# Performance work log

Hardware: AMD Instinct MI355X
Metric: run time of the kernel (lower is better)

## Reference

```python
import jax, jax.numpy as jnp
import numpy as np

B, N, CS, CV, K = 8, 2048, 256, 128, 3
EPS = 1e-6


def _eq_layernorm(s, v):
    # scalars: standard layernorm over channels; vectors: RMS of channel norms (equivariant)
    mu = s.mean(-1, keepdims=True)
    var = ((s - mu) ** 2).mean(-1, keepdims=True)
    s = (s - mu) * jax.lax.rsqrt(var + EPS)
    n2 = (v ** 2).sum(-1).mean(-1, keepdims=True)  # [b,n,1]
    v = v * jax.lax.rsqrt(n2 + EPS)[..., None]
    return s, v


def setup_inputs() -> dict:
    key = jax.random.key(0)
    ks = jax.random.split(key, 7)
    fan_s = K * (CS + CV)       # 1152
    fan_v = K * (CS + 2 * CV)   # 1536
    return {
        "x_s": jax.random.normal(ks[0], (B, N, CS), jnp.float32),
        "x_v": jax.random.normal(ks[1], (B, N, CV, 3), jnp.float32),
        "coords": jax.random.normal(ks[2], (B, N, 3), jnp.float32) * 10.0,
        "W_conv_s": jax.random.normal(ks[3], (fan_s, CS), jnp.float32),
        "W_conv_v": jax.random.normal(ks[4], (fan_v, CV), jnp.float32),
        "W_si_s": jax.random.normal(ks[5], (CS, CS), jnp.float32),
        "W_si_v": jax.random.normal(ks[6], (CV, CV), jnp.float32),
    }


def reference(x_s, x_v, coords, W_conv_s, W_conv_v, W_si_s, W_si_v):
    b, n, cs = x_s.shape
    cv = x_v.shape[2]
    pad = K // 2
    # 'same' padding: zeros for features, edge for coords (zero displacement at boundary)
    sp = jnp.pad(x_s, ((0, 0), (pad, pad), (0, 0)))
    vp = jnp.pad(x_v, ((0, 0), (pad, pad), (0, 0), (0, 0)))
    cp = jnp.pad(coords, ((0, 0), (pad, pad), (0, 0)), mode="edge")
    s_win = jnp.stack([sp[:, k:k + n] for k in range(K)], 2)   # [b,n,K,cs]
    v_win = jnp.stack([vp[:, k:k + n] for k in range(K)], 2)   # [b,n,K,cv,3]
    c_win = jnp.stack([cp[:, k:k + n] for k in range(K)], 2)   # [b,n,K,3]

    d = c_win - coords[:, :, None, :]
    dn = jnp.linalg.norm(d, axis=-1, keepdims=True)
    rhat = d * jnp.where(dn > 1e-6, 1.0 / jnp.maximum(dn, 1e-6), 0.0)

    # Clebsch-Gordan paths of (0e,1e) features with sh = (1, rhat)
    vdot = jnp.einsum("bnkcd,bnkd->bnkc", v_win, rhat)                    # 1x1 -> 0
    scal_in = jnp.concatenate([s_win, vdot], -1).reshape(b, n, -1)        # [b,n,K*(cs+cv)]
    s_rhat = s_win[..., None] * rhat[:, :, :, None, :]                    # 0x1 -> 1
    v_cross = jnp.cross(v_win, rhat[:, :, :, None, :])                    # 1x1 -> 1
    vec_in = jnp.concatenate([v_win, s_rhat, v_cross], 3).reshape(b, n, -1, 3)

    # SequenceConvolution linear mixing (fan-in normalized) + norm=True
    h_s = jnp.einsum("bnp,po->bno", scal_in, W_conv_s) / float(np.sqrt(scal_in.shape[-1]))
    h_v = jnp.einsum("bnpd,po->bnod", vec_in, W_conv_v) / float(np.sqrt(vec_in.shape[2]))
    h_s, h_v = _eq_layernorm(h_s, h_v)

    # SelfInteraction: per-degree channel mixing, residual=True, norm_last=True
    y_s = h_s + h_s @ W_si_s / float(np.sqrt(cs))
    y_v = h_v + jnp.einsum("bncd,co->bnod", h_v, W_si_v) / float(np.sqrt(cv))
    y_s, y_v = _eq_layernorm(y_s, y_v)

    # block Residual + final EquivariantLayerNorm
    z_s, z_v = _eq_layernorm(x_s + y_s, x_v + y_v)
    return z_s, z_v
```

## Files before the change

kernel.cpp:

```cpp
#include <hip/hip_runtime.h>
#include <hip/hip_bf16.h>


typedef __attribute__((ext_vector_type(8))) short short8;
typedef __attribute__((ext_vector_type(4))) short short4v;
typedef __attribute__((ext_vector_type(4))) float f32x4;
typedef unsigned short u16;

#define B_   8
#define N_   2048
#define EPS_ 1e-6f
#define TB   32

#define OFF_CS 0
#define OFF_V  294912
#define OFF_G  393216
#define OFF_SS 491520
#define OFF_SV 557056

#define MFMA(a,b,c) __builtin_amdgcn_mfma_f32_16x16x32_bf16((a),(b),(c),0,0,0)

__device__ __forceinline__ u16 f2b(float v){ __hip_bfloat16 h=__float2bfloat16(v); return *(u16*)&h; }

__global__ __launch_bounds__(256) void prep_weights(
    const float* __restrict__ Wcs, const float* __restrict__ Wcv,
    const float* __restrict__ Wss, const float* __restrict__ Wsv,
    u16* __restrict__ ws)
{
    const int bid = blockIdx.x;
    const float* src; int N, r0, ld, c0; u16* dst; int tile;
    if (bid < 288)      { src=Wcs; N=256; r0=0; dst=ws+OFF_CS; ld=1152; c0=0; tile=bid; }
    else if (bid < 336) { int k=(bid-288)/16; tile=(bid-288)%16;
                          src=Wcv; N=128; r0=k*512;     dst=ws+OFF_V; ld=768; c0=k*256; }
    else if (bid < 432) { int k=(bid-336)/32; tile=(bid-336)%32;
                          src=Wcv; N=128; r0=k*512+128; dst=ws+OFF_G; ld=768; c0=k*256; }
    else if (bid < 480) { int k=(bid-432)/16; tile=(bid-432)%16;
                          src=Wcv; N=128; r0=k*512+384; dst=ws+OFF_V; ld=768; c0=k*256+128; }
    else if (bid < 544) { tile=bid-480; src=Wss; N=256; r0=0; dst=ws+OFF_SS; ld=256; c0=0; }
    else                { tile=bid-544; src=Wsv; N=128; r0=0; dst=ws+OFF_SV; ld=128; c0=0; }
    const int ntN = N >> 5;
    const int kt = (tile/ntN)*32, nn = (tile%ntN)*32;
    __shared__ float t[32][33];
    const int r = threadIdx.x >> 5, c = threadIdx.x & 31;
#pragma unroll
    for (int i = 0; i < 4; ++i)
        t[r+8*i][c] = src[(size_t)(r0+kt+r+8*i)*N + nn+c];
    __syncthreads();
#pragma unroll
    for (int i = 0; i < 4; ++i)
        dst[(size_t)(nn+r+8*i)*ld + c0+kt+c] = f2b(t[c][r+8*i]);
}

__device__ __forceinline__ void ln_reduce8(
    float p1[2][4], float p2[2][4], float pv[2][4], f32x4* red,
    int lm, int lq4, int w, float mu[2][4], float ss[2][4], float vs[2][4])
{
    __syncthreads();
#pragma unroll
    for (int m2 = 1; m2 < 16; m2 <<= 1)
#pragma unroll
        for (int m = 0; m < 2; ++m)
#pragma unroll
            for (int q = 0; q < 4; ++q) {
                p1[m][q] += __shfl_xor(p1[m][q], m2);
                p2[m][q] += __shfl_xor(p2[m][q], m2);
                pv[m][q] += __shfl_xor(pv[m][q], m2);
            }
    if (lm == 0)
#pragma unroll
        for (int m = 0; m < 2; ++m)
#pragma unroll
            for (int q = 0; q < 4; ++q) {
                f32x4 r = {p1[m][q], p2[m][q], pv[m][q], 0.f};
                red[(m*16+lq4+q)*8 + w] = r;
            }
    __syncthreads();
#pragma unroll
    for (int m = 0; m < 2; ++m)
#pragma unroll
        for (int q = 0; q < 4; ++q) {
            const int t = m*16 + lq4 + q;
            f32x4 rs = red[t*8+0];
#pragma unroll
            for (int i = 1; i < 8; ++i) rs += red[t*8+i];
            const float mm = rs.x * (1.f/256.f);
            mu[m][q] = mm;
            ss[m][q] = rsqrtf(rs.y*(1.f/256.f) - mm*mm + EPS_);
            vs[m][q] = rsqrtf(rs.z*(1.f/128.f) + EPS_);
        }
}

__global__ __launch_bounds__(512, 2) void mixing_main(
    const float* __restrict__ x_s, const float* __restrict__ x_v,
    const float* __restrict__ coords, const u16* __restrict__ wt,
    float* __restrict__ out)
{
    __shared__ __align__(16) char smem[81408];
    u16* fs  = (u16*)smem;
    u16* fv  = (u16*)(smem + 25088);
    u16* hsb = (u16*)smem;
    u16* hvb = (u16*)(smem + 25088);
    float* xvL = (float*)(smem + 25088);
    float* rhp = (float*)(smem + 75776);
    f32x4* red = (f32x4*)(smem + 77312);

    const int tid = threadIdx.x;
    const int w   = tid >> 6, l = tid & 63;
    const int lm  = l & 15, lk8 = (l >> 4) << 3, lq4 = (l >> 4) << 2;
    const int gt0 = blockIdx.x * TB;
    const int n0  = gt0 & (N_ - 1);
    const int seq0 = gt0 - n0;
    const size_t ZV0 = (size_t)B_ * N_ * 256;

    if (tid < 96) {
        const int t = tid / 3, k = tid - 3 * (tid / 3);
        const int jn = n0 + t + k - 1;
        const int jc = jn < 0 ? 0 : (jn > N_-1 ? N_-1 : jn);
        const float* cj = coords + (size_t)(seq0 + jc) * 3;
        const float* c0p = coords + (size_t)(gt0 + t) * 3;
        const float d0 = cj[0]-c0p[0], d1 = cj[1]-c0p[1], d2 = cj[2]-c0p[2];
        const float dn = sqrtf(d0*d0 + d1*d1 + d2*d2);
        const float inv = dn > 1e-6f ? 1.f/dn : 0.f;
        rhp[(t*3+k)*4+0] = d0*inv; rhp[(t*3+k)*4+1] = d1*inv; rhp[(t*3+k)*4+2] = d2*inv;
    }
    __syncthreads();

    const f32x4 fz = {0.f,0.f,0.f,0.f};
    f32x4 acc_s[2][2] = {{fz,fz},{fz,fz}};
    f32x4 accv[6] = {fz,fz,fz,fz,fz,fz};
    f32x4 agc[2] = {fz, fz};

    const int bt = tid >> 4;
    const int bx = tid & 15;

#pragma unroll
    for (int k = 0; k < 3; ++k) {
        const int jn = n0 + bt + k - 1;
        const bool valid = (unsigned)jn < (unsigned)N_;
        const size_t j = (size_t)seq0 + (valid ? jn : 0);
        {
            const int c0 = bx * 16;
            float v[16];
            if (valid) {
                const float4* sp = (const float4*)(x_s + j*256 + c0);
#pragma unroll
                for (int i = 0; i < 4; ++i) {
                    float4 f = sp[i];
                    v[4*i]=f.x; v[4*i+1]=f.y; v[4*i+2]=f.z; v[4*i+3]=f.w;
                }
            } else {
#pragma unroll
                for (int i = 0; i < 16; ++i) v[i] = 0.f;
            }
            short8 p0, p1;
#pragma unroll
            for (int i = 0; i < 8; ++i) { p0[i]=(short)f2b(v[i]); p1[i]=(short)f2b(v[8+i]); }
            *(short8*)(fs + bt*392 + c0)     = p0;
            *(short8*)(fs + bt*392 + c0 + 8) = p1;
        }
        {
            const int c0 = bx * 8;
            const float r0 = rhp[(bt*3+k)*4+0];
            const float r1 = rhp[(bt*3+k)*4+1];
            const float r2 = rhp[(bt*3+k)*4+2];
#pragma unroll
            for (int hh = 0; hh < 2; ++hh) {
                float vv[12];
                if (valid) {
                    const float4* vp = (const float4*)(x_v + ((size_t)j*128 + c0 + 4*hh)*3);
#pragma unroll
                    for (int i = 0; i < 3; ++i) {
                        float4 f = vp[i];
                        vv[4*i]=f.x; vv[4*i+1]=f.y; vv[4*i+2]=f.z; vv[4*i+3]=f.w;
                    }
                } else {
#pragma unroll
                    for (int i = 0; i < 12; ++i) vv[i] = 0.f;
                }
                short4v dv, w0, w1, w2, x0, x1, x2;
#pragma unroll
                for (int m = 0; m < 4; ++m) {
                    const float a0 = vv[3*m], a1 = vv[3*m+1], a2 = vv[3*m+2];
                    dv[m] = (short)f2b(a0*r0 + a1*r1 + a2*r2);
                    w0[m] = (short)f2b(a0); w1[m] = (short)f2b(a1); w2[m] = (short)f2b(a2);
                    x0[m] = (short)f2b(a1*r2 - a2*r1);
                    x1[m] = (short)f2b(a2*r0 - a0*r2);
                    x2[m] = (short)f2b(a0*r1 - a1*r0);
                }
                const int cc = c0 + 4*hh;
                *(short4v*)(fs + bt*392 + 256 + cc)          = dv;
                *(short4v*)(fv + (0*32+bt)*264 + cc)         = w0;
                *(short4v*)(fv + (1*32+bt)*264 + cc)         = w1;
                *(short4v*)(fv + (2*32+bt)*264 + cc)         = w2;
                *(short4v*)(fv + (0*32+bt)*264 + 128 + cc)   = x0;
                *(short4v*)(fv + (1*32+bt)*264 + 128 + cc)   = x1;
                *(short4v*)(fv + (2*32+bt)*264 + 128 + cc)   = x2;
            }
        }

        const u16* bS0 = wt + OFF_CS + k*384 + (size_t)((2*w+0)*16+lm)*1152;
        const u16* bS1 = wt + OFF_CS + k*384 + (size_t)((2*w+1)*16+lm)*1152;
        const u16* bGp = wt + OFF_G  + k*256 + (size_t)(w*16+lm)*768;
        const u16* bVp = wt + OFF_V  + k*256 + (size_t)(w*16+lm)*768;
        short8 Bs0[3], Bs1[3], Bg[3], Bv[4];
#pragma unroll
        for (int i = 0; i < 3; ++i) {
            Bs0[i] = *(const short8*)(bS0 + i*32 + lk8);
            Bs1[i] = *(const short8*)(bS1 + i*32 + lk8);
            Bg[i]  = *(const short8*)(bGp + i*32 + lk8);
        }
        __syncthreads();

#pragma unroll
        for (int ks = 0; ks < 12; ++ks) {
            const int r = ks % 3;
            const short8 b0 = Bs0[r], b1 = Bs1[r], bg = Bg[r];
            if (ks + 3 < 12) {
                Bs0[r] = *(const short8*)(bS0 + (ks+3)*32 + lk8);
                Bs1[r] = *(const short8*)(bS1 + (ks+3)*32 + lk8);
            }
            if (ks + 3 < 8)
                Bg[r] = *(const short8*)(bGp + (ks+3)*32 + lk8);
            if (ks == 9) {
#pragma unroll
                for (int i = 0; i < 4; ++i)
                    Bv[i] = *(const short8*)(bVp + i*32 + lk8);
            }
            const int ko = ks*32 + lk8;
            const short8 a0 = *(const short8*)(fs + lm*392 + ko);
            const short8 a1 = *(const short8*)(fs + (16+lm)*392 + ko);
            acc_s[0][0] = MFMA(a0, b0, acc_s[0][0]);
            acc_s[1][0] = MFMA(a1, b0, acc_s[1][0]);
            acc_s[0][1] = MFMA(a0, b1, acc_s[0][1]);
            acc_s[1][1] = MFMA(a1, b1, acc_s[1][1]);
            if (ks < 8) {
                agc[0] = MFMA(a0, bg, agc[0]);
                agc[1] = MFMA(a1, bg, agc[1]);
            }
        }
#pragma unroll
        for (int ks = 0; ks < 8; ++ks) {
            const int r = ks & 3;
            const short8 bv = Bv[r];
            if (ks + 4 < 8)
                Bv[r] = *(const short8*)(bVp + (ks+4)*32 + lk8);
            const int ko = ks*32 + lk8;
#pragma unroll
            for (int mi = 0; mi < 6; ++mi) {
                const short8 a = *(const short8*)(fv + (mi*16+lm)*264 + ko);
                accv[mi] = MFMA(a, bv, accv[mi]);
            }
        }
#pragma unroll
        for (int mi = 0; mi < 6; ++mi) {
            const int m = mi & 1, d = mi >> 1;
#pragma unroll
            for (int q = 0; q < 4; ++q)
                accv[mi][q] += agc[m][q] * rhp[((m*16+lq4+q)*3 + k)*4 + d];
        }
        agc[0] = fz; agc[1] = fz;
        __syncthreads();
    }

    const float inv_fs = 0.029462783f;
    const float inv_fv = 0.0255155136f;
#pragma unroll
    for (int m = 0; m < 2; ++m)
#pragma unroll
        for (int u = 0; u < 2; ++u)
#pragma unroll
            for (int q = 0; q < 4; ++q) acc_s[m][u][q] *= inv_fs;
#pragma unroll
    for (int mi = 0; mi < 6; ++mi)
#pragma unroll
        for (int q = 0; q < 4; ++q) accv[mi][q] *= inv_fv;

    float p1[2][4], p2[2][4], pv[2][4], mu[2][4], ss[2][4], vs[2][4];
#pragma unroll
    for (int m = 0; m < 2; ++m)
#pragma unroll
        for (int q = 0; q < 4; ++q) {
            float a = 0.f, b = 0.f, c = 0.f;
#pragma unroll
            for (int u = 0; u < 2; ++u) { const float x = acc_s[m][u][q]; a += x; b += x*x; }
#pragma unroll
            for (int d = 0; d < 3; ++d) { const float x = accv[d*2+m][q]; c += x*x; }
            p1[m][q] = a; p2[m][q] = b; pv[m][q] = c;
        }
    ln_reduce8(p1, p2, pv, red, lm, lq4, w, mu, ss, vs);

#pragma unroll
    for (int m = 0; m < 2; ++m)
#pragma unroll
        for (int u = 0; u < 2; ++u)
#pragma unroll
            for (int q = 0; q < 4; ++q) {
                const float h = (acc_s[m][u][q] - mu[m][q]) * ss[m][q];
                acc_s[m][u][q] = h;
                hsb[(m*16+lq4+q)*264 + (2*w+u)*16 + lm] = f2b(h);
            }
#pragma unroll
    for (int mi = 0; mi < 6; ++mi)
#pragma unroll
        for (int q = 0; q < 4; ++q) {
            const float h = accv[mi][q] * vs[mi&1][q];
            accv[mi][q] = h;
            hvb[(mi*16+lq4+q)*136 + w*16 + lm] = f2b(h);
        }

    const u16* bP0 = wt + OFF_SS + (size_t)((2*w+0)*16+lm)*256;
    const u16* bP1 = wt + OFF_SS + (size_t)((2*w+1)*16+lm)*256;
    const u16* bPv = wt + OFF_SV + (size_t)(w*16+lm)*128;
    short8 Cs0[3], Cs1[3], Cv[4];
#pragma unroll
    for (int i = 0; i < 3; ++i) {
        Cs0[i] = *(const short8*)(bP0 + i*32 + lk8);
        Cs1[i] = *(const short8*)(bP1 + i*32 + lk8);
    }
#pragma unroll
    for (int i = 0; i < 4; ++i)
        Cv[i] = *(const short8*)(bPv + i*32 + lk8);
    __syncthreads();

    f32x4 accs[2][2] = {{fz,fz},{fz,fz}};
    f32x4 accw[6] = {fz,fz,fz,fz,fz,fz};
#pragma unroll
    for (int ks = 0; ks < 8; ++ks) {
        const int r = ks % 3;
        const short8 c0 = Cs0[r], c1 = Cs1[r];
        if (ks + 3 < 8) {
            Cs0[r] = *(const short8*)(bP0 + (ks+3)*32 + lk8);
            Cs1[r] = *(const short8*)(bP1 + (ks+3)*32 + lk8);
        }
        const int ko = ks*32 + lk8;
        const short8 a0 = *(const short8*)(hsb + lm*264 + ko);
        const short8 a1 = *(const short8*)(hsb + (16+lm)*264 + ko);
        accs[0][0] = MFMA(a0, c0, accs[0][0]);
        accs[1][0] = MFMA(a1, c0, accs[1][0]);
        accs[0][1] = MFMA(a0, c1, accs[0][1]);
        accs[1][1] = MFMA(a1, c1, accs[1][1]);
    }
#pragma unroll
    for (int ks = 0; ks < 4; ++ks) {
        const int ko = ks*32 + lk8;
#pragma unroll
        for (int mi = 0; mi < 6; ++mi) {
            const short8 a = *(const short8*)(hvb + (mi*16+lm)*136 + ko);
            accw[mi] = MFMA(a, Cv[ks], accw[mi]);
        }
    }

#pragma unroll
    for (int m = 0; m < 2; ++m)
#pragma unroll
        for (int u = 0; u < 2; ++u)
#pragma unroll
            for (int q = 0; q < 4; ++q) acc_s[m][u][q] += accs[m][u][q] * 0.0625f;
#pragma unroll
    for (int mi = 0; mi < 6; ++mi)
#pragma unroll
        for (int q = 0; q < 4; ++q) accv[mi][q] += accw[mi][q] * 0.08838834764f;

#pragma unroll
    for (int m = 0; m < 2; ++m)
#pragma unroll
        for (int q = 0; q < 4; ++q) {
            float a = 0.f, b = 0.f, c = 0.f;
#pragma unroll
            for (int u = 0; u < 2; ++u) { const float x = acc_s[m][u][q]; a += x; b += x*x; }
#pragma unroll
            for (int d = 0; d < 3; ++d) { const float x = accv[d*2+m][q]; c += x*x; }
            p1[m][q] = a; p2[m][q] = b; pv[m][q] = c;
        }
    float4 xr[6];
    {
        const float4* xvsrc = (const float4*)(x_v + (size_t)gt0 * 384);
#pragma unroll
        for (int i = 0; i < 6; ++i) xr[i] = xvsrc[tid + i*512];
    }
    ln_reduce8(p1, p2, pv, red, lm, lq4, w, mu, ss, vs);
#pragma unroll
    for (int i = 0; i < 6; ++i) ((float4*)xvL)[tid + i*512] = xr[i];
    __syncthreads();

#pragma unroll
    for (int m = 0; m < 2; ++m)
#pragma unroll
        for (int u = 0; u < 2; ++u)
#pragma unroll
            for (int q = 0; q < 4; ++q)
                acc_s[m][u][q] = (acc_s[m][u][q] - mu[m][q]) * ss[m][q]
                    + x_s[(size_t)(gt0 + m*16 + lq4 + q)*256 + (2*w+u)*16 + lm];
#pragma unroll
    for (int mi = 0; mi < 6; ++mi)
#pragma unroll
        for (int q = 0; q < 4; ++q) {
            const int t = (mi&1)*16 + lq4 + q;
            accv[mi][q] = accv[mi][q] * vs[mi&1][q]
                + xvL[t*384 + (w*16+lm)*3 + (mi>>1)];
        }

#pragma unroll
    for (int m = 0; m < 2; ++m)
#pragma unroll
        for (int q = 0; q < 4; ++q) {
            float a = 0.f, b = 0.f, c = 0.f;
#pragma unroll
            for (int u = 0; u < 2; ++u) { const float x = acc_s[m][u][q]; a += x; b += x*x; }
#pragma unroll
            for (int d = 0; d < 3; ++d) { const float x = accv[d*2+m][q]; c += x*x; }
            p1[m][q] = a; p2[m][q] = b; pv[m][q] = c;
        }
    ln_reduce8(p1, p2, pv, red, lm, lq4, w, mu, ss, vs);

#pragma unroll
    for (int m = 0; m < 2; ++m)
#pragma unroll
        for (int u = 0; u < 2; ++u)
#pragma unroll
            for (int q = 0; q < 4; ++q)
                out[(size_t)(gt0 + m*16 + lq4 + q)*256 + (2*w+u)*16 + lm] =
                    (acc_s[m][u][q] - mu[m][q]) * ss[m][q];
#pragma unroll
    for (int mi = 0; mi < 6; ++mi)
#pragma unroll
        for (int q = 0; q < 4; ++q) {
            const int t = (mi&1)*16 + lq4 + q;
            xvL[t*384 + (w*16+lm)*3 + (mi>>1)] = accv[mi][q] * vs[mi&1][q];
        }
    __syncthreads();
    {
        f32x4* dst = (f32x4*)(out + ZV0 + (size_t)gt0 * 384);
        const f32x4* srcv = (const f32x4*)xvL;
#pragma unroll
        for (int i = 0; i < 6; ++i)
            __builtin_nontemporal_store(srcv[tid + i*512], dst + tid + i*512);
    }
}

extern "C" void kernel_launch(void* const* d_in, const int* in_sizes, int n_in,
                              void* d_out, int out_size, void* d_ws, size_t ws_size,
                              hipStream_t stream) {
    const float* x_s    = (const float*)d_in[0];
    const float* x_v    = (const float*)d_in[1];
    const float* coords = (const float*)d_in[2];
    const float* Wcs    = (const float*)d_in[3];
    const float* Wcv    = (const float*)d_in[4];
    const float* Wss    = (const float*)d_in[5];
    const float* Wsv    = (const float*)d_in[6];
    float* out = (float*)d_out;
    u16* ws = (u16*)d_ws;

    hipLaunchKernelGGL(prep_weights, dim3(560), dim3(256), 0, stream,
                       Wcs, Wcv, Wss, Wsv, ws);
    hipLaunchKernelGGL(mixing_main, dim3((B_ * N_) / TB), dim3(512), 0, stream,
                       x_s, x_v, coords, ws, out);
}
```

Baseline: 125.5 us.

## Double per-block token tile to 64 rows to reuse weight fragments across more MFMAs

Raises the token tile per block from 32 to 64. Each wave now issues four 16-row MFMA M-tiles per loaded weight fragment instead of two, which halves global weight traffic per token and the number of blocks. In exchange it doubles LDS use to about 159 KB and roughly doubles accumulator registers. With launch bounds still asking for 2 blocks of 512 threads, this likely drops occupancy to one block per CU and risks register spills. The k loop is also no longer unrolled.

```diff
diff --git a/kernel.cpp b/kernel.cpp
--- a/kernel.cpp
+++ b/kernel.cpp
@@ -3,14 +3,13 @@
 
 
 typedef __attribute__((ext_vector_type(8))) short short8;
-typedef __attribute__((ext_vector_type(4))) short short4v;
 typedef __attribute__((ext_vector_type(4))) float f32x4;
 typedef unsigned short u16;
 
 #define B_   8
 #define N_   2048
 #define EPS_ 1e-6f
-#define TB   32
+#define TB   64
 
 #define OFF_CS 0
 #define OFF_V  294912
@@ -51,15 +50,15 @@
         dst[(size_t)(nn+r+8*i)*ld + c0+kt+c] = f2b(t[c][r+8*i]);
 }
 
-__device__ __forceinline__ void ln_reduce8(
-    float p1[2][4], float p2[2][4], float pv[2][4], f32x4* red,
-    int lm, int lq4, int w, float mu[2][4], float ss[2][4], float vs[2][4])
+__device__ __forceinline__ void ln_reduce(
+    float p1[4][4], float p2[4][4], float pv[4][4], f32x4* red,
+    int lm, int lq4, int w, float mu[4][4], float ss[4][4], float vs[4][4])
 {
     __syncthreads();
 #pragma unroll
     for (int m2 = 1; m2 < 16; m2 <<= 1)
 #pragma unroll
-        for (int m = 0; m < 2; ++m)
+        for (int m = 0; m < 4; ++m)
 #pragma unroll
             for (int q = 0; q < 4; ++q) {
                 p1[m][q] += __shfl_xor(p1[m][q], m2);
@@ -68,7 +67,7 @@
             }
     if (lm == 0)
 #pragma unroll
-        for (int m = 0; m < 2; ++m)
+        for (int m = 0; m < 4; ++m)
 #pragma unroll
             for (int q = 0; q < 4; ++q) {
                 f32x4 r = {p1[m][q], p2[m][q], pv[m][q], 0.f};
@@ -76,7 +75,7 @@
             }
     __syncthreads();
 #pragma unroll
-    for (int m = 0; m < 2; ++m)
+    for (int m = 0; m < 4; ++m)
 #pragma unroll
         for (int q = 0; q < 4; ++q) {
             const int t = m*16 + lq4 + q;
@@ -95,14 +94,14 @@
     const float* __restrict__ coords, const u16* __restrict__ wt,
     float* __restrict__ out)
 {
-    __shared__ __align__(16) char smem[81408];
-    u16* fs  = (u16*)smem;
-    u16* fv  = (u16*)(smem + 25088);
-    u16* hsb = (u16*)smem;
-    u16* hvb = (u16*)(smem + 25088);
-    float* xvL = (float*)(smem + 25088);
-    float* rhp = (float*)(smem + 75776);
-    f32x4* red = (f32x4*)(smem + 77312);
+    __shared__ __align__(16) char smem[162816];
+    u16*   fs  = (u16*)smem;
+    u16*   fv  = (u16*)(smem + 50176);
+    u16*   hsb = (u16*)smem;
+    u16*   hvb = (u16*)(smem + 50176);
+    float* xvL = (float*)(smem + 50176);
+    float* rhp = (float*)(smem + 151552);
+    f32x4* red = (f32x4*)(smem + 154624);
 
     const int tid = threadIdx.x;
     const int w   = tid >> 6, l = tid & 63;
@@ -112,7 +111,7 @@
     const int seq0 = gt0 - n0;
     const size_t ZV0 = (size_t)B_ * N_ * 256;
 
-    if (tid < 96) {
+    if (tid < 192) {
         const int t = tid / 3, k = tid - 3 * (tid / 3);
         const int jn = n0 + t + k - 1;
         const int jc = jn < 0 ? 0 : (jn > N_-1 ? N_-1 : jn);
@@ -126,60 +125,64 @@
     __syncthreads();
 
     const f32x4 fz = {0.f,0.f,0.f,0.f};
-    f32x4 acc_s[2][2] = {{fz,fz},{fz,fz}};
-    f32x4 accv[6] = {fz,fz,fz,fz,fz,fz};
-    f32x4 agc[2] = {fz, fz};
-
-    const int bt = tid >> 4;
-    const int bx = tid & 15;
-
-#pragma unroll
+    f32x4 acc_s[4][2];
+    f32x4 accv[12];
+#pragma unroll
+    for (int m = 0; m < 4; ++m) { acc_s[m][0] = fz; acc_s[m][1] = fz; }
+#pragma unroll
+    for (int mi = 0; mi < 12; ++mi) accv[mi] = fz;
+
+    const int bt = tid >> 3;
+    const int bx = tid & 7;
+
+#pragma unroll 1
     for (int k = 0; k < 3; ++k) {
         const int jn = n0 + bt + k - 1;
         const bool valid = (unsigned)jn < (unsigned)N_;
         const size_t j = (size_t)seq0 + (valid ? jn : 0);
         {
-            const int c0 = bx * 16;
-            float v[16];
-            if (valid) {
-                const float4* sp = (const float4*)(x_s + j*256 + c0);
-#pragma unroll
-                for (int i = 0; i < 4; ++i) {
-                    float4 f = sp[i];
-                    v[4*i]=f.x; v[4*i+1]=f.y; v[4*i+2]=f.z; v[4*i+3]=f.w;
+            const int c0 = bx * 32;
+            const float4* sp = (const float4*)(x_s + j*256 + c0);
+#pragma unroll
+            for (int h = 0; h < 4; ++h) {
+                float v[8];
+                if (valid) {
+                    const float4 f0 = sp[2*h], f1 = sp[2*h+1];
+                    v[0]=f0.x; v[1]=f0.y; v[2]=f0.z; v[3]=f0.w;
+                    v[4]=f1.x; v[5]=f1.y; v[6]=f1.z; v[7]=f1.w;
+                } else {
+#pragma unroll
+                    for (int i = 0; i < 8; ++i) v[i] = 0.f;
                 }
-            } else {
-#pragma unroll
-                for (int i = 0; i < 16; ++i) v[i] = 0.f;
-            }
-            short8 p0, p1;
-#pragma unroll
-            for (int i = 0; i < 8; ++i) { p0[i]=(short)f2b(v[i]); p1[i]=(short)f2b(v[8+i]); }
-            *(short8*)(fs + bt*392 + c0)     = p0;
-            *(short8*)(fs + bt*392 + c0 + 8) = p1;
+                short8 p;
+#pragma unroll
+                for (int i = 0; i < 8; ++i) p[i] = (short)f2b(v[i]);
+                *(short8*)(fs + bt*392 + c0 + 8*h) = p;
+            }
         }
         {
-            const int c0 = bx * 8;
+            const int ch0 = bx * 16;
             const float r0 = rhp[(bt*3+k)*4+0];
             const float r1 = rhp[(bt*3+k)*4+1];
             const float r2 = rhp[(bt*3+k)*4+2];
 #pragma unroll
             for (int hh = 0; hh < 2; ++hh) {
-                float vv[12];
+                const int cb = ch0 + 8*hh;
+                float vv[24];
                 if (valid) {
-                    const float4* vp = (const float4*)(x_v + ((size_t)j*128 + c0 + 4*hh)*3);
-#pragma unroll
-                    for (int i = 0; i < 3; ++i) {
-                        float4 f = vp[i];
+                    const float4* vp = (const float4*)(x_v + ((size_t)j*128 + cb)*3);
+#pragma unroll
+                    for (int i = 0; i < 6; ++i) {
+                        const float4 f = vp[i];
                         vv[4*i]=f.x; vv[4*i+1]=f.y; vv[4*i+2]=f.z; vv[4*i+3]=f.w;
                     }
                 } else {
 #pragma unroll
-                    for (int i = 0; i < 12; ++i) vv[i] = 0.f;
+                    for (int i = 0; i < 24; ++i) vv[i] = 0.f;
                 }
-                short4v dv, w0, w1, w2, x0, x1, x2;
-#pragma unroll
-                for (int m = 0; m < 4; ++m) {
+                short8 dv, w0, w1, w2, x0, x1, x2;
+#pragma unroll
+                for (int m = 0; m < 8; ++m) {
                     const float a0 = vv[3*m], a1 = vv[3*m+1], a2 = vv[3*m+2];
                     dv[m] = (short)f2b(a0*r0 + a1*r1 + a2*r2);
                     w0[m] = (short)f2b(a0); w1[m] = (short)f2b(a1); w2[m] = (short)f2b(a2);
@@ -187,14 +190,13 @@
                     x1[m] = (short)f2b(a2*r0 - a0*r2);
                     x2[m] = (short)f2b(a0*r1 - a1*r0);
                 }
-                const int cc = c0 + 4*hh;
-                *(short4v*)(fs + bt*392 + 256 + cc)          = dv;
-                *(short4v*)(fv + (0*32+bt)*264 + cc)         = w0;
-                *(short4v*)(fv + (1*32+bt)*264 + cc)         = w1;
-                *(short4v*)(fv + (2*32+bt)*264 + cc)         = w2;
-                *(short4v*)(fv + (0*32+bt)*264 + 128 + cc)   = x0;
-                *(short4v*)(fv + (1*32+bt)*264 + 128 + cc)   = x1;
-                *(short4v*)(fv + (2*32+bt)*264 + 128 + cc)   = x2;
+                *(short8*)(fs + bt*392 + 256 + cb)            = dv;
+                *(short8*)(fv + (0*64+bt)*264 + cb)           = w0;
+                *(short8*)(fv + (1*64+bt)*264 + cb)           = w1;
+                *(short8*)(fv + (2*64+bt)*264 + cb)           = w2;
+                *(short8*)(fv + (0*64+bt)*264 + 128 + cb)     = x0;
+                *(short8*)(fv + (1*64+bt)*264 + 128 + cb)     = x1;
+                *(short8*)(fv + (2*64+bt)*264 + 128 + cb)     = x2;
             }
         }
 
@@ -211,6 +213,7 @@
         }
         __syncthreads();
 
+        f32x4 agc[4] = {fz, fz, fz, fz};
 #pragma unroll
         for (int ks = 0; ks < 12; ++ks) {
             const int r = ks % 3;
@@ -227,15 +230,12 @@
                     Bv[i] = *(const short8*)(bVp + i*32 + lk8);
             }
             const int ko = ks*32 + lk8;
-            const short8 a0 = *(const short8*)(fs + lm*392 + ko);
-            const short8 a1 = *(const short8*)(fs + (16+lm)*392 + ko);
-            acc_s[0][0] = MFMA(a0, b0, acc_s[0][0]);
-            acc_s[1][0] = MFMA(a1, b0, acc_s[1][0]);
-            acc_s[0][1] = MFMA(a0, b1, acc_s[0][1]);
-            acc_s[1][1] = MFMA(a1, b1, acc_s[1][1]);
-            if (ks < 8) {
-                agc[0] = MFMA(a0, bg, agc[0]);
-                agc[1] = MFMA(a1, bg, agc[1]);
+#pragma unroll
+            for (int m = 0; m < 4; ++m) {
+                const short8 a = *(const short8*)(fs + (m*16+lm)*392 + ko);
+                acc_s[m][0] = MFMA(a, b0, acc_s[m][0]);
+                acc_s[m][1] = MFMA(a, b1, acc_s[m][1]);
+                if (ks < 8) agc[m] = MFMA(a, bg, agc[m]);
             }
         }
 #pragma unroll
@@ -246,51 +246,51 @@
                 Bv[r] = *(const short8*)(bVp + (ks+4)*32 + lk8);
             const int ko = ks*32 + lk8;
 #pragma unroll
-            for (int mi = 0; mi < 6; ++mi) {
-                const short8 a = *(const short8*)(fv + (mi*16+lm)*264 + ko);
+            for (int mi = 0; mi < 12; ++mi) {
+                const short8 a = *(const short8*)(
+                    fv + ((mi>>2)*64 + (mi&3)*16 + lm)*264 + ko);
                 accv[mi] = MFMA(a, bv, accv[mi]);
             }
         }
 #pragma unroll
-        for (int mi = 0; mi < 6; ++mi) {
-            const int m = mi & 1, d = mi >> 1;
+        for (int mi = 0; mi < 12; ++mi) {
+            const int m = mi & 3, d = mi >> 2;
 #pragma unroll
             for (int q = 0; q < 4; ++q)
                 accv[mi][q] += agc[m][q] * rhp[((m*16+lq4+q)*3 + k)*4 + d];
         }
-        agc[0] = fz; agc[1] = fz;
         __syncthreads();
     }
 
     const float inv_fs = 0.029462783f;
     const float inv_fv = 0.0255155136f;
 #pragma unroll
-    for (int m = 0; m < 2; ++m)
+    for (int m = 0; m < 4; ++m)
 #pragma unroll
         for (int u = 0; u < 2; ++u)
 #pragma unroll
             for (int q = 0; q < 4; ++q) acc_s[m][u][q] *= inv_fs;
 #pragma unroll
-    for (int mi = 0; mi < 6; ++mi)
+    for (int mi = 0; mi < 12; ++mi)
 #pragma unroll
         for (int q = 0; q < 4; ++q) accv[mi][q] *= inv_fv;
 
-    float p1[2][4], p2[2][4], pv[2][4], mu[2][4], ss[2][4], vs[2][4];
-#pragma unroll
-    for (int m = 0; m < 2; ++m)
+    float p1[4][4], p2[4][4], pv[4][4], mu[4][4], ss[4][4], vs[4][4];
+#pragma unroll
+    for (int m = 0; m < 4; ++m)
 #pragma unroll
         for (int q = 0; q < 4; ++q) {
             float a = 0.f, b = 0.f, c = 0.f;
 #pragma unroll
             for (int u = 0; u < 2; ++u) { const float x = acc_s[m][u][q]; a += x; b += x*x; }
 #pragma unroll
-            for (int d = 0; d < 3; ++d) { const float x = accv[d*2+m][q]; c += x*x; }
+            for (int d = 0; d < 3; ++d) { const float x = accv[d*4+m][q]; c += x*x; }
             p1[m][q] = a; p2[m][q] = b; pv[m][q] = c;
         }
-    ln_reduce8(p1, p2, pv, red, lm, lq4, w, mu, ss, vs);
-
-#pragma unroll
-    for (int m = 0; m < 2; ++m)
+    ln_reduce(p1, p2, pv, red, lm, lq4, w, mu, ss, vs);
+
+#pragma unroll
+    for (int m = 0; m < 4; ++m)
 #pragma unroll
         for (int u = 0; u < 2; ++u)
 #pragma unroll
@@ -300,12 +300,12 @@
                 hsb[(m*16+lq4+q)*264 + (2*w+u)*16 + lm] = f2b(h);
             }
 #pragma unroll
-    for (int mi = 0; mi < 6; ++mi)
-#pragma unroll
-        for (int q = 0; q < 4; ++q) {
-            const float h = accv[mi][q] * vs[mi&1][q];
+    for (int mi = 0; mi < 12; ++mi)
+#pragma unroll
+        for (int q = 0; q < 4; ++q) {
+            const float h = accv[mi][q] * vs[mi&3][q];
             accv[mi][q] = h;
-            hvb[(mi*16+lq4+q)*136 + w*16 + lm] = f2b(h);
+            hvb[((mi>>2)*64 + (mi&3)*16 + lq4 + q)*136 + w*16 + lm] = f2b(h);
         }
 
     const u16* bP0 = wt + OFF_SS + (size_t)((2*w+0)*16+lm)*256;
@@ -322,8 +322,12 @@
         Cv[i] = *(const short8*)(bPv + i*32 + lk8);
     __syncthreads();
 
-    f32x4 accs[2][2] = {{fz,fz},{fz,fz}};
-    f32x4 accw[6] = {fz,fz,fz,fz,fz,fz};
+    f32x4 accs[4][2];
+    f32x4 accw[12];
+#pragma unroll
+    for (int m = 0; m < 4; ++m) { accs[m][0] = fz; accs[m][1] = fz; }
+#pragma unroll
+    for (int mi = 0; mi < 12; ++mi) accw[mi] = fz;
 #pragma unroll
     for (int ks = 0; ks < 8; ++ks) {
         const int r = ks % 3;
@@ -333,58 +337,59 @@
             Cs1[r] = *(const short8*)(bP1 + (ks+3)*32 + lk8);
         }
         const int ko = ks*32 + lk8;
-        const short8 a0 = *(const short8*)(hsb + lm*264 + ko);
-        const short8 a1 = *(const short8*)(hsb + (16+lm)*264 + ko);
-        accs[0][0] = MFMA(a0, c0, accs[0][0]);
-        accs[1][0] = MFMA(a1, c0, accs[1][0]);
-        accs[0][1] = MFMA(a0, c1, accs[0][1]);
-        accs[1][1] = MFMA(a1, c1, accs[1][1]);
+#pragma unroll
+        for (int m = 0; m < 4; ++m) {
+            const short8 a = *(const short8*)(hsb + (m*16+lm)*264 + ko);
+            accs[m][0] = MFMA(a, c0, accs[m][0]);
+            accs[m][1] = MFMA(a, c1, accs[m][1]);
+        }
     }
 #pragma unroll
     for (int ks = 0; ks < 4; ++ks) {
         const int ko = ks*32 + lk8;
 #pragma unroll
-        for (int mi = 0; mi < 6; ++mi) {
-            const short8 a = *(const short8*)(hvb + (mi*16+lm)*136 + ko);
+        for (int mi = 0; mi < 12; ++mi) {
+            const short8 a = *(const short8*)(
+                hvb + ((mi>>2)*64 + (mi&3)*16 + lm)*136 + ko);
             accw[mi] = MFMA(a, Cv[ks], accw[mi]);
         }
     }
 
 #pragma unroll
-    for (int m = 0; m < 2; ++m)
+    for (int m = 0; m < 4; ++m)
 #pragma unroll
         for (int u = 0; u < 2; ++u)
 #pragma unroll
             for (int q = 0; q < 4; ++q) acc_s[m][u][q] += accs[m][u][q] * 0.0625f;
 #pragma unroll
-    for (int mi = 0; mi < 6; ++mi)
+    for (int mi = 0; mi < 12; ++mi)
 #pragma unroll
         for (int q = 0; q < 4; ++q) accv[mi][q] += accw[mi][q] * 0.08838834764f;
 
 #pragma unroll
-    for (int m = 0; m < 2; ++m)
+    for (int m = 0; m < 4; ++m)
 #pragma unroll
         for (int q = 0; q < 4; ++q) {
             float a = 0.f, b = 0.f, c = 0.f;
 #pragma unroll
             for (int u = 0; u < 2; ++u) { const float x = acc_s[m][u][q]; a += x; b += x*x; }
 #pragma unroll
-            for (int d = 0; d < 3; ++d) { const float x = accv[d*2+m][q]; c += x*x; }
+            for (int d = 0; d < 3; ++d) { const float x = accv[d*4+m][q]; c += x*x; }
             p1[m][q] = a; p2[m][q] = b; pv[m][q] = c;
         }
-    float4 xr[6];
+    float4 xr[12];
     {
         const float4* xvsrc = (const float4*)(x_v + (size_t)gt0 * 384);
 #pragma unroll
-        for (int i = 0; i < 6; ++i) xr[i] = xvsrc[tid + i*512];
-    }
-    ln_reduce8(p1, p2, pv, red, lm, lq4, w, mu, ss, vs);
-#pragma unroll
-    for (int i = 0; i < 6; ++i) ((float4*)xvL)[tid + i*512] = xr[i];
-    __syncthreads();
-
-#pragma unroll
-    for (int m = 0; m < 2; ++m)
+        for (int i = 0; i < 12; ++i) xr[i] = xvsrc[tid + i*512];
+    }
+    ln_reduce(p1, p2, pv, red, lm, lq4, w, mu, ss, vs);
+#pragma unroll
+    for (int i = 0; i < 12; ++i) ((float4*)xvL)[tid + i*512] = xr[i];
+    __syncthreads();
+
+#pragma unroll
+    for (int m = 0; m < 4; ++m)
 #pragma unroll
         for (int u = 0; u < 2; ++u)
 #pragma unroll
@@ -392,29 +397,29 @@
                 acc_s[m][u][q] = (acc_s[m][u][q] - mu[m][q]) * ss[m][q]
                     + x_s[(size_t)(gt0 + m*16 + lq4 + q)*256 + (2*w+u)*16 + lm];
 #pragma unroll
-    for (int mi = 0; mi < 6; ++mi)
-#pragma unroll
-        for (int q = 0; q < 4; ++q) {
-            const int t = (mi&1)*16 + lq4 + q;
-            accv[mi][q] = accv[mi][q] * vs[mi&1][q]
-                + xvL[t*384 + (w*16+lm)*3 + (mi>>1)];
-        }
-
-#pragma unroll
-    for (int m = 0; m < 2; ++m)
+    for (int mi = 0; mi < 12; ++mi)
+#pragma unroll
+        for (int q = 0; q < 4; ++q) {
+            const int t = (mi&3)*16 + lq4 + q;
+            accv[mi][q] = accv[mi][q] * vs[mi&3][q]
+                + xvL[t*384 + (w*16+lm)*3 + (mi>>2)];
+        }
+
+#pragma unroll
+    for (int m = 0; m < 4; ++m)
 #pragma unroll
         for (int q = 0; q < 4; ++q) {
             float a = 0.f, b = 0.f, c = 0.f;
 #pragma unroll
             for (int u = 0; u < 2; ++u) { const float x = acc_s[m][u][q]; a += x; b += x*x; }
 #pragma unroll
-            for (int d = 0; d < 3; ++d) { const float x = accv[d*2+m][q]; c += x*x; }
+            for (int d = 0; d < 3; ++d) { const float x = accv[d*4+m][q]; c += x*x; }
             p1[m][q] = a; p2[m][q] = b; pv[m][q] = c;
         }
-    ln_reduce8(p1, p2, pv, red, lm, lq4, w, mu, ss, vs);
-
-#pragma unroll
-    for (int m = 0; m < 2; ++m)
+    ln_reduce(p1, p2, pv, red, lm, lq4, w, mu, ss, vs);
+
+#pragma unroll
+    for (int m = 0; m < 4; ++m)
 #pragma unroll
         for (int u = 0; u < 2; ++u)
 #pragma unroll
@@ -422,18 +427,18 @@
                 out[(size_t)(gt0 + m*16 + lq4 + q)*256 + (2*w+u)*16 + lm] =
                     (acc_s[m][u][q] - mu[m][q]) * ss[m][q];
 #pragma unroll
-    for (int mi = 0; mi < 6; ++mi)
-#pragma unroll
-        for (int q = 0; q < 4; ++q) {
-            const int t = (mi&1)*16 + lq4 + q;
-            xvL[t*384 + (w*16+lm)*3 + (mi>>1)] = accv[mi][q] * vs[mi&1][q];
+    for (int mi = 0; mi < 12; ++mi)
+#pragma unroll
+        for (int q = 0; q < 4; ++q) {
+            const int t = (mi&3)*16 + lq4 + q;
+            xvL[t*384 + (w*16+lm)*3 + (mi>>2)] = accv[mi][q] * vs[mi&3][q];
         }
     __syncthreads();
     {
         f32x4* dst = (f32x4*)(out + ZV0 + (size_t)gt0 * 384);
         const f32x4* srcv = (const f32x4*)xvL;
 #pragma unroll
-        for (int i = 0; i < 6; ++i)
+        for (int i = 0; i < 12; ++i)
             __builtin_nontemporal_store(srcv[tid + i*512], dst + tid + i*512);
     }
 }
```

Result: faster. 111.8 us (-10.9%).
